# Kernel optimization log

Hardware: AMD Instinct MI355X
Metric: run time of the kernel (lower is better)

Reference implementation:

```python
import jax, jax.numpy as jnp
import numpy as np

N_NODES = 100000
N_HYPEREDGES = 10000
NNZ = 1600000

def setup_inputs() -> dict:
    key = jax.random.key(0)
    k = jax.random.split(key, 7)
    return {
        "x": jax.random.normal(k[0], (N_NODES, 1), dtype=jnp.float32),
        "W1": jax.random.normal(k[1], (1, 128), dtype=jnp.float32) * 0.5,
        "b1": jax.random.normal(k[2], (128,), dtype=jnp.float32) * 0.1,
        "W2": jax.random.normal(k[3], (128, 1), dtype=jnp.float32) * 0.1,
        "b2": jax.random.normal(k[4], (1,), dtype=jnp.float32) * 0.1,
        "node_idx": jax.random.randint(k[5], (NNZ,), 0, N_NODES, dtype=jnp.int64),
        "edge_idx": jax.random.randint(k[6], (NNZ,), 0, N_HYPEREDGES, dtype=jnp.int64),
    }

def _hypergraph_conv(x, W, b, node_idx, edge_idx, n_nodes, n_edges):
    # PyG HypergraphConv (use_attention=False, hyperedge_weight=1):
    # out = D^-1 H B^-1 H^T (X W) + b
    x = x @ W  # [N, F_out]
    ones = jnp.ones(node_idx.shape[0], dtype=x.dtype)
    D = jax.ops.segment_sum(ones, node_idx, num_segments=n_nodes)   # node degree
    B = jax.ops.segment_sum(ones, edge_idx, num_segments=n_edges)   # hyperedge degree
    D_inv = jnp.where(D > 0, 1.0 / D, 0.0)
    B_inv = jnp.where(B > 0, 1.0 / B, 0.0)
    # node -> hyperedge: e = B^-1 H^T x
    e = B_inv[:, None] * jax.ops.segment_sum(x[node_idx], edge_idx, num_segments=n_edges)
    # hyperedge -> node: out = D^-1 H e
    out = D_inv[:, None] * jax.ops.segment_sum(e[edge_idx], node_idx, num_segments=n_nodes)
    return out + b

def reference(x, W1, b1, W2, b2, node_idx, edge_idx):
    n_nodes = x.shape[0]
    h = _hypergraph_conv(x, W1, b1, node_idx, edge_idx, n_nodes, N_HYPEREDGES)
    h = jax.nn.relu(h)
    out = _hypergraph_conv(h, W2, b2, node_idx, edge_idx, n_nodes, N_HYPEREDGES)
    return out
```

## Files before the change

kernel.cpp:

```cpp
#include <hip/hip_runtime.h>

static constexpr int N_NODES = 100000;
static constexpr int N_EDGES = 10000;
static constexpr int NNZ     = 1600000;

static constexpr int G1    = 256;
static constexpr int CHUNK = NNZ / G1;
static constexpr int NRN   = 250;
static constexpr int RN    = 400;
static constexpr int NRE   = 250;
static constexpr int RE    = 40;
static constexpr int SLOT  = 64;
static constexpr int BLK   = 1024;
static constexpr int NW    = BLK / 64;
static constexpr int GF    = 250;
static constexpr int NBAR  = 8;
static constexpr int BARSTRIDE = 32;


__device__ __forceinline__ float ld_a(const float* p) {
    return __hip_atomic_load(p, __ATOMIC_RELAXED, __HIP_MEMORY_SCOPE_AGENT);
}
__device__ __forceinline__ void st_a(float* p, float v) {
    __hip_atomic_store(p, v, __ATOMIC_RELAXED, __HIP_MEMORY_SCOPE_AGENT);
}

__device__ __forceinline__ void grid_barrier(unsigned* bar, int phase) {
    __syncthreads();
    if (threadIdx.x == 0) {
        unsigned* cnt = bar + (size_t)phase * NBAR * BARSTRIDE;
        __hip_atomic_fetch_add(cnt + (blockIdx.x & (NBAR - 1)) * BARSTRIDE, 1u,
                               __ATOMIC_RELAXED, __HIP_MEMORY_SCOPE_AGENT);
        unsigned sum;
        do {
            __builtin_amdgcn_s_sleep(2);
            sum = 0u;
            #pragma unroll
            for (int g = 0; g < NBAR; ++g)
                sum += __hip_atomic_load(cnt + g * BARSTRIDE,
                                         __ATOMIC_RELAXED, __HIP_MEMORY_SCOPE_AGENT);
        } while (sum < (unsigned)GF);
    }
    __syncthreads();
}

__global__ __launch_bounds__(BLK) void k_bin(
        const int* __restrict__ nidx, const int* __restrict__ eidx,
        unsigned* __restrict__ binN, unsigned* __restrict__ binE,
        unsigned* __restrict__ cntN, unsigned* __restrict__ cntE,
        unsigned* __restrict__ bar) {
    __shared__ unsigned cN[NRN], cE[NRE];
    if (blockIdx.x == 0 && threadIdx.x < 3 * NBAR * BARSTRIDE) bar[threadIdx.x] = 0u;
    for (int j = threadIdx.x; j < NRN; j += BLK) cN[j] = 0u;
    for (int j = threadIdx.x; j < NRE; j += BLK) cE[j] = 0u;
    __syncthreads();
    const int b = blockIdx.x;
    const int i0 = b * CHUNK, i1 = i0 + CHUNK;
    for (int i = i0 + threadIdx.x; i < i1; i += BLK) {
        int n = nidx[i], e = eidx[i];
        int rn = n / RN;
        int re = e / RE;
        unsigned pn = atomicAdd(&cN[rn], 1u);
        unsigned pe = atomicAdd(&cE[re], 1u);
        binN[((size_t)rn * G1 + b) * SLOT + pn] = ((unsigned)(n - rn * RN) << 14) | (unsigned)e;
        binE[((size_t)re * G1 + b) * SLOT + pe] = ((unsigned)(e - re * RE) << 17) | (unsigned)n;
    }
    __syncthreads();
    for (int j = threadIdx.x; j < NRN; j += BLK) cntN[(size_t)j * G1 + b] = cN[j];
    for (int j = threadIdx.x; j < NRE; j += BLK) cntE[(size_t)j * G1 + b] = cE[j];
}

__global__ __launch_bounds__(BLK) void k_fused(
        const unsigned* __restrict__ binN, const unsigned* __restrict__ binE,
        const unsigned* __restrict__ cntN, const unsigned* __restrict__ cntE,
        const float* __restrict__ x,
        const float* __restrict__ W1, const float* __restrict__ b1,
        const float* __restrict__ W2, const float* __restrict__ b2,
        float* __restrict__ v1, float* __restrict__ v2, float* __restrict__ y,
        unsigned* __restrict__ bar, float* __restrict__ out) {
    __shared__ union {
        struct { unsigned scnt[G1]; float sS[NW][RE]; unsigned sC[NW][RE]; } e;
        struct { float sV[N_EDGES]; float sS[RN]; unsigned sC[RN]; unsigned scnt[G1];
                 float wgt[384]; } n;
    } sm;
    const int b = blockIdx.x;
    const int t = threadIdx.x;

    float my_binv = 0.0f;
    float my_dinv = 0.0f;

    {
        for (int j = t; j < NW * RE; j += BLK) { (&sm.e.sS[0][0])[j] = 0.0f; (&sm.e.sC[0][0])[j] = 0u; }
        if (t < G1) sm.e.scnt[t] = cntE[(size_t)b * G1 + t];
        __syncthreads();
        const int wv = t >> 6;
        const unsigned* base = binE + (size_t)b * G1 * SLOT;
        for (int j = t; j < G1 * SLOT; j += BLK) {
            int s = j & (SLOT - 1), bb = j >> 6;
            if ((unsigned)s < sm.e.scnt[bb]) {
                unsigned w = base[j];
                atomicAdd(&sm.e.sS[wv][w >> 17], x[w & 0x1FFFFu]);
                atomicAdd(&sm.e.sC[wv][w >> 17], 1u);
            }
        }
        __syncthreads();
        if (t < RE) {
            float s = 0.0f; unsigned c = 0u;
            #pragma unroll
            for (int k = 0; k < NW; ++k) { s += sm.e.sS[k][t]; c += sm.e.sC[k][t]; }
            my_binv = (c > 0u) ? (1.0f / (float)c) : 0.0f;
            st_a(&v1[b * RE + t], s * my_binv);
        }
    }
    grid_barrier(bar, 0);

    {
        for (int j = t; j < N_EDGES; j += BLK) sm.n.sV[j] = ld_a(&v1[j]);
        if (t < RN) { sm.n.sS[t] = 0.0f; sm.n.sC[t] = 0u; }
        if (t < G1) sm.n.scnt[t] = cntN[(size_t)b * G1 + t];
        if (t < 128) {
            sm.n.wgt[t]       = W1[t];
            sm.n.wgt[128 + t] = b1[t];
            sm.n.wgt[256 + t] = W2[t];
        }
        __syncthreads();
        const unsigned* base = binN + (size_t)b * G1 * SLOT;
        for (int j = t; j < G1 * SLOT; j += BLK) {
            int s = j & (SLOT - 1), bb = j >> 6;
            if ((unsigned)s < sm.n.scnt[bb]) {
                unsigned w = base[j];
                unsigned nl = w >> 14;
                atomicAdd(&sm.n.sS[nl], sm.n.sV[w & 0x3FFFu]);
                atomicAdd(&sm.n.sC[nl], 1u);
            }
        }
        __syncthreads();
        if (t < RN) {
            unsigned c = sm.n.sC[t];
            my_dinv = (c > 0u) ? (1.0f / (float)c) : 0.0f;
            float tt = sm.n.sS[t] * my_dinv;
            float acc = 0.0f;
            #pragma unroll
            for (int f = 0; f < 128; ++f) {
                float h = fmaf(tt, sm.n.wgt[f], sm.n.wgt[128 + f]);
                h = fmaxf(h, 0.0f);
                acc = fmaf(h, sm.n.wgt[256 + f], acc);
            }
            st_a(&y[b * RN + t], acc);
        }
    }
    grid_barrier(bar, 1);

    {
        for (int j = t; j < NW * RE; j += BLK) (&sm.e.sS[0][0])[j] = 0.0f;
        if (t < G1) sm.e.scnt[t] = cntE[(size_t)b * G1 + t];
        __syncthreads();
        const int wv = t >> 6;
        const unsigned* base = binE + (size_t)b * G1 * SLOT;
        for (int j = t; j < G1 * SLOT; j += BLK) {
            int s = j & (SLOT - 1), bb = j >> 6;
            if ((unsigned)s < sm.e.scnt[bb]) {
                unsigned w = base[j];
                atomicAdd(&sm.e.sS[wv][w >> 17], ld_a(&y[w & 0x1FFFFu]));
            }
        }
        __syncthreads();
        if (t < RE) {
            float s = 0.0f;
            #pragma unroll
            for (int k = 0; k < NW; ++k) s += sm.e.sS[k][t];
            st_a(&v2[b * RE + t], s * my_binv);
        }
    }
    grid_barrier(bar, 2);

    {
        for (int j = t; j < N_EDGES; j += BLK) sm.n.sV[j] = ld_a(&v2[j]);
        if (t < RN) sm.n.sS[t] = 0.0f;
        if (t < G1) sm.n.scnt[t] = cntN[(size_t)b * G1 + t];
        __syncthreads();
        const unsigned* base = binN + (size_t)b * G1 * SLOT;
        for (int j = t; j < G1 * SLOT; j += BLK) {
            int s = j & (SLOT - 1), bb = j >> 6;
            if ((unsigned)s < sm.n.scnt[bb]) {
                unsigned w = base[j];
                atomicAdd(&sm.n.sS[w >> 14], sm.n.sV[w & 0x3FFFu]);
            }
        }
        __syncthreads();
        if (t < RN) {
            out[b * RN + t] = fmaf(sm.n.sS[t], my_dinv, b2[0]);
        }
    }
}

extern "C" void kernel_launch(void* const* d_in, const int* in_sizes, int n_in,
                              void* d_out, int out_size, void* d_ws, size_t ws_size,
                              hipStream_t stream) {
    const float* x    = (const float*)d_in[0];
    const float* W1   = (const float*)d_in[1];
    const float* b1   = (const float*)d_in[2];
    const float* W2   = (const float*)d_in[3];
    const float* b2   = (const float*)d_in[4];
    const int*   nidx = (const int*)d_in[5];
    const int*   eidx = (const int*)d_in[6];
    float*       out  = (float*)d_out;

    char* ws = (char*)d_ws;
    unsigned* binN = (unsigned*)(ws + 0);
    unsigned* binE = (unsigned*)(ws + 16384000);
    unsigned* cntN = (unsigned*)(ws + 32768000);
    unsigned* cntE = (unsigned*)(ws + 33024000);
    float*    v1   = (float*)(ws + 33280000);
    float*    y    = (float*)(ws + 33320000);
    float*    v2   = (float*)(ws + 33720000);
    unsigned* bar  = (unsigned*)(ws + 33760000);

    k_bin  <<<G1, BLK, 0, stream>>>(nidx, eidx, binN, binE, cntN, cntE, bar);
    k_fused<<<GF, BLK, 0, stream>>>(binN, binE, cntN, cntE, x, W1, b1, W2, b2,
                                    v1, v2, y, bar, out);
}
```

Before: 88.46 us.

## Compute layer-2 edge sums from node-side partials and split barrier arrive/wait

The layer-2 node-to-edge aggregation no longer reads y from global memory through the edge bins. Each block now scatters its local y values into a per-block partial array over all 10000 edges in shared memory, writes it to global memory, and after a barrier each block reduces its 40 edges' partials across the 250 blocks. The grid barrier is split into an arrive step and a wait step, so setup work overlaps the wait, and a single master block sets a flag that the other blocks poll. This avoids the random global gathers of y, at the cost of a 10 MB partial-sum write and read and a serialized flag-based release.

```diff
diff --git a/kernel.cpp b/kernel.cpp
--- a/kernel.cpp
+++ b/kernel.cpp
@@ -12,10 +12,8 @@
 static constexpr int RE    = 40;
 static constexpr int SLOT  = 64;
 static constexpr int BLK   = 1024;
-static constexpr int NW    = BLK / 64;
+static constexpr int NW    = 16;
 static constexpr int GF    = 250;
-static constexpr int NBAR  = 8;
-static constexpr int BARSTRIDE = 32;
 
 
 __device__ __forceinline__ float ld_a(const float* p) {
@@ -25,21 +23,32 @@
     __hip_atomic_store(p, v, __ATOMIC_RELAXED, __HIP_MEMORY_SCOPE_AGENT);
 }
 
-__device__ __forceinline__ void grid_barrier(unsigned* bar, int phase) {
-    __syncthreads();
+__device__ __forceinline__ void bar_arrive(unsigned* bar, int phase) {
+    __syncthreads();
+    if (threadIdx.x == 0)
+        __hip_atomic_fetch_add(bar + phase * 256 + (blockIdx.x & 7) * 32, 1u,
+                               __ATOMIC_RELAXED, __HIP_MEMORY_SCOPE_AGENT);
+}
+__device__ __forceinline__ void bar_wait(unsigned* bar, int phase) {
     if (threadIdx.x == 0) {
-        unsigned* cnt = bar + (size_t)phase * NBAR * BARSTRIDE;
-        __hip_atomic_fetch_add(cnt + (blockIdx.x & (NBAR - 1)) * BARSTRIDE, 1u,
-                               __ATOMIC_RELAXED, __HIP_MEMORY_SCOPE_AGENT);
-        unsigned sum;
-        do {
-            __builtin_amdgcn_s_sleep(2);
-            sum = 0u;
-            #pragma unroll
-            for (int g = 0; g < NBAR; ++g)
-                sum += __hip_atomic_load(cnt + g * BARSTRIDE,
-                                         __ATOMIC_RELAXED, __HIP_MEMORY_SCOPE_AGENT);
-        } while (sum < (unsigned)GF);
+        unsigned* flag = bar + 768 + phase * 32;
+        if (blockIdx.x == 0) {
+            unsigned* cnt = bar + phase * 256;
+            unsigned sum;
+            do {
+                __builtin_amdgcn_s_sleep(2);
+                sum = 0u;
+                #pragma unroll
+                for (int g = 0; g < 8; ++g)
+                    sum += __hip_atomic_load(cnt + g * 32, __ATOMIC_RELAXED,
+                                             __HIP_MEMORY_SCOPE_AGENT);
+            } while (sum < (unsigned)GF);
+            __hip_atomic_store(flag, 1u, __ATOMIC_RELAXED, __HIP_MEMORY_SCOPE_AGENT);
+        } else {
+            while (__hip_atomic_load(flag, __ATOMIC_RELAXED,
+                                     __HIP_MEMORY_SCOPE_AGENT) == 0u)
+                __builtin_amdgcn_s_sleep(2);
+        }
     }
     __syncthreads();
 }
@@ -50,7 +59,7 @@
         unsigned* __restrict__ cntN, unsigned* __restrict__ cntE,
         unsigned* __restrict__ bar) {
     __shared__ unsigned cN[NRN], cE[NRE];
-    if (blockIdx.x == 0 && threadIdx.x < 3 * NBAR * BARSTRIDE) bar[threadIdx.x] = 0u;
+    if (blockIdx.x == 0 && threadIdx.x < 896) bar[threadIdx.x] = 0u;
     for (int j = threadIdx.x; j < NRN; j += BLK) cN[j] = 0u;
     for (int j = threadIdx.x; j < NRE; j += BLK) cE[j] = 0u;
     __syncthreads();
@@ -76,122 +85,126 @@
         const float* __restrict__ x,
         const float* __restrict__ W1, const float* __restrict__ b1,
         const float* __restrict__ W2, const float* __restrict__ b2,
-        float* __restrict__ v1, float* __restrict__ v2, float* __restrict__ y,
+        float* __restrict__ v1, float* __restrict__ v2, float* __restrict__ P_S,
         unsigned* __restrict__ bar, float* __restrict__ out) {
-    __shared__ union {
-        struct { unsigned scnt[G1]; float sS[NW][RE]; unsigned sC[NW][RE]; } e;
-        struct { float sV[N_EDGES]; float sS[RN]; unsigned sC[RN]; unsigned scnt[G1];
-                 float wgt[384]; } n;
-    } sm;
+    __shared__ float    sBig[N_EDGES];
+    __shared__ float    eS[NW][RE];
+    __shared__ unsigned eC[NW][RE];
+    __shared__ float    sS_n[RN];
+    __shared__ unsigned sC_n[RN];
+    __shared__ unsigned scntE[G1];
+    __shared__ unsigned scntN[G1];
+    __shared__ float    wgt[384];
+    __shared__ float    y_loc[RN];
+
     const int b = blockIdx.x;
     const int t = threadIdx.x;
-
+    const int wv = t >> 6;
     float my_binv = 0.0f;
     float my_dinv = 0.0f;
 
+    for (int j = t; j < NW * RE; j += BLK) { (&eS[0][0])[j] = 0.0f; (&eC[0][0])[j] = 0u; }
+    if (t < G1) scntE[t] = cntE[(size_t)b * G1 + t];
+    __syncthreads();
     {
-        for (int j = t; j < NW * RE; j += BLK) { (&sm.e.sS[0][0])[j] = 0.0f; (&sm.e.sC[0][0])[j] = 0u; }
-        if (t < G1) sm.e.scnt[t] = cntE[(size_t)b * G1 + t];
-        __syncthreads();
-        const int wv = t >> 6;
-        const unsigned* base = binE + (size_t)b * G1 * SLOT;
+        const unsigned* baseE = binE + (size_t)b * G1 * SLOT;
         for (int j = t; j < G1 * SLOT; j += BLK) {
             int s = j & (SLOT - 1), bb = j >> 6;
-            if ((unsigned)s < sm.e.scnt[bb]) {
-                unsigned w = base[j];
-                atomicAdd(&sm.e.sS[wv][w >> 17], x[w & 0x1FFFFu]);
-                atomicAdd(&sm.e.sC[wv][w >> 17], 1u);
+            if ((unsigned)s < scntE[bb]) {
+                unsigned w = baseE[j];
+                atomicAdd(&eS[wv][w >> 17], x[w & 0x1FFFFu]);
+                atomicAdd(&eC[wv][w >> 17], 1u);
             }
         }
         __syncthreads();
         if (t < RE) {
             float s = 0.0f; unsigned c = 0u;
             #pragma unroll
-            for (int k = 0; k < NW; ++k) { s += sm.e.sS[k][t]; c += sm.e.sC[k][t]; }
+            for (int k = 0; k < NW; ++k) { s += eS[k][t]; c += eC[k][t]; }
             my_binv = (c > 0u) ? (1.0f / (float)c) : 0.0f;
             st_a(&v1[b * RE + t], s * my_binv);
         }
     }
-    grid_barrier(bar, 0);
-
+    bar_arrive(bar, 0);
+    if (t < RN) { sS_n[t] = 0.0f; sC_n[t] = 0u; }
+    if (t < G1) scntN[t] = cntN[(size_t)b * G1 + t];
+    if (t < 128) { wgt[t] = W1[t]; wgt[128 + t] = b1[t]; wgt[256 + t] = W2[t]; }
+    bar_wait(bar, 0);
+
+    const unsigned* baseN = binN + (size_t)b * G1 * SLOT;
+    for (int j = t; j < N_EDGES; j += BLK) sBig[j] = ld_a(&v1[j]);
+    __syncthreads();
+    for (int j = t; j < G1 * SLOT; j += BLK) {
+        int s = j & (SLOT - 1), bb = j >> 6;
+        if ((unsigned)s < scntN[bb]) {
+            unsigned w = baseN[j];
+            atomicAdd(&sS_n[w >> 14], sBig[w & 0x3FFFu]);
+            atomicAdd(&sC_n[w >> 14], 1u);
+        }
+    }
+    __syncthreads();
+    if (t < RN) {
+        unsigned c = sC_n[t];
+        my_dinv = (c > 0u) ? (1.0f / (float)c) : 0.0f;
+        float tt = sS_n[t] * my_dinv;
+        float acc = 0.0f;
+        #pragma unroll
+        for (int f = 0; f < 128; ++f) {
+            float h = fmaf(tt, wgt[f], wgt[128 + f]);
+            h = fmaxf(h, 0.0f);
+            acc = fmaf(h, wgt[256 + f], acc);
+        }
+        y_loc[t] = acc;
+    }
+    __syncthreads();
+    for (int j = t; j < N_EDGES; j += BLK) sBig[j] = 0.0f;
+    __syncthreads();
+    for (int j = t; j < G1 * SLOT; j += BLK) {
+        int s = j & (SLOT - 1), bb = j >> 6;
+        if ((unsigned)s < scntN[bb]) {
+            unsigned w = baseN[j];
+            atomicAdd(&sBig[w & 0x3FFFu], y_loc[w >> 14]);
+        }
+    }
+    __syncthreads();
     {
-        for (int j = t; j < N_EDGES; j += BLK) sm.n.sV[j] = ld_a(&v1[j]);
-        if (t < RN) { sm.n.sS[t] = 0.0f; sm.n.sC[t] = 0u; }
-        if (t < G1) sm.n.scnt[t] = cntN[(size_t)b * G1 + t];
-        if (t < 128) {
-            sm.n.wgt[t]       = W1[t];
-            sm.n.wgt[128 + t] = b1[t];
-            sm.n.wgt[256 + t] = W2[t];
-        }
-        __syncthreads();
-        const unsigned* base = binN + (size_t)b * G1 * SLOT;
-        for (int j = t; j < G1 * SLOT; j += BLK) {
-            int s = j & (SLOT - 1), bb = j >> 6;
-            if ((unsigned)s < sm.n.scnt[bb]) {
-                unsigned w = base[j];
-                unsigned nl = w >> 14;
-                atomicAdd(&sm.n.sS[nl], sm.n.sV[w & 0x3FFFu]);
-                atomicAdd(&sm.n.sC[nl], 1u);
-            }
-        }
-        __syncthreads();
-        if (t < RN) {
-            unsigned c = sm.n.sC[t];
-            my_dinv = (c > 0u) ? (1.0f / (float)c) : 0.0f;
-            float tt = sm.n.sS[t] * my_dinv;
+        float* ps = P_S + (size_t)b * N_EDGES;
+        for (int j = t; j < N_EDGES; j += BLK) st_a(&ps[j], sBig[j]);
+    }
+    bar_arrive(bar, 1);
+    bar_wait(bar, 1);
+
+    {
+        const int lane = t & 63;
+        if (lane < RE) {
             float acc = 0.0f;
-            #pragma unroll
-            for (int f = 0; f < 128; ++f) {
-                float h = fmaf(tt, sm.n.wgt[f], sm.n.wgt[128 + f]);
-                h = fmaxf(h, 0.0f);
-                acc = fmaf(h, sm.n.wgt[256 + f], acc);
-            }
-            st_a(&y[b * RN + t], acc);
-        }
-    }
-    grid_barrier(bar, 1);
-
-    {
-        for (int j = t; j < NW * RE; j += BLK) (&sm.e.sS[0][0])[j] = 0.0f;
-        if (t < G1) sm.e.scnt[t] = cntE[(size_t)b * G1 + t];
-        __syncthreads();
-        const int wv = t >> 6;
-        const unsigned* base = binE + (size_t)b * G1 * SLOT;
-        for (int j = t; j < G1 * SLOT; j += BLK) {
-            int s = j & (SLOT - 1), bb = j >> 6;
-            if ((unsigned)s < sm.e.scnt[bb]) {
-                unsigned w = base[j];
-                atomicAdd(&sm.e.sS[wv][w >> 17], ld_a(&y[w & 0x1FFFFu]));
-            }
-        }
-        __syncthreads();
-        if (t < RE) {
-            float s = 0.0f;
-            #pragma unroll
-            for (int k = 0; k < NW; ++k) s += sm.e.sS[k][t];
-            st_a(&v2[b * RE + t], s * my_binv);
-        }
-    }
-    grid_barrier(bar, 2);
-
-    {
-        for (int j = t; j < N_EDGES; j += BLK) sm.n.sV[j] = ld_a(&v2[j]);
-        if (t < RN) sm.n.sS[t] = 0.0f;
-        if (t < G1) sm.n.scnt[t] = cntN[(size_t)b * G1 + t];
-        __syncthreads();
-        const unsigned* base = binN + (size_t)b * G1 * SLOT;
-        for (int j = t; j < G1 * SLOT; j += BLK) {
-            int s = j & (SLOT - 1), bb = j >> 6;
-            if ((unsigned)s < sm.n.scnt[bb]) {
-                unsigned w = base[j];
-                atomicAdd(&sm.n.sS[w >> 14], sm.n.sV[w & 0x3FFFu]);
-            }
-        }
-        __syncthreads();
-        if (t < RN) {
-            out[b * RN + t] = fmaf(sm.n.sS[t], my_dinv, b2[0]);
-        }
-    }
+            for (int g = wv; g < GF; g += NW)
+                acc += ld_a(&P_S[(size_t)g * N_EDGES + b * RE + lane]);
+            eS[wv][lane] = acc;
+        }
+    }
+    __syncthreads();
+    if (t < RE) {
+        float s = 0.0f;
+        #pragma unroll
+        for (int k = 0; k < NW; ++k) s += eS[k][t];
+        st_a(&v2[b * RE + t], s * my_binv);
+    }
+    bar_arrive(bar, 2);
+    if (t < RN) sS_n[t] = 0.0f;
+    bar_wait(bar, 2);
+
+    for (int j = t; j < N_EDGES; j += BLK) sBig[j] = ld_a(&v2[j]);
+    __syncthreads();
+    for (int j = t; j < G1 * SLOT; j += BLK) {
+        int s = j & (SLOT - 1), bb = j >> 6;
+        if ((unsigned)s < scntN[bb]) {
+            unsigned w = baseN[j];
+            atomicAdd(&sS_n[w >> 14], sBig[w & 0x3FFFu]);
+        }
+    }
+    __syncthreads();
+    if (t < RN) out[b * RN + t] = fmaf(sS_n[t], my_dinv, b2[0]);
 }
 
 extern "C" void kernel_launch(void* const* d_in, const int* in_sizes, int n_in,
@@ -212,11 +225,11 @@
     unsigned* cntN = (unsigned*)(ws + 32768000);
     unsigned* cntE = (unsigned*)(ws + 33024000);
     float*    v1   = (float*)(ws + 33280000);
-    float*    y    = (float*)(ws + 33320000);
-    float*    v2   = (float*)(ws + 33720000);
-    unsigned* bar  = (unsigned*)(ws + 33760000);
+    float*    v2   = (float*)(ws + 33320000);
+    float*    P_S  = (float*)(ws + 33360000);
+    unsigned* bar  = (unsigned*)(ws + 43360000);
 
     k_bin  <<<G1, BLK, 0, stream>>>(nidx, eidx, binN, binE, cntN, cntE, bar);
     k_fused<<<GF, BLK, 0, stream>>>(binN, binE, cntN, cntE, x, W1, b1, W2, b2,
-                                    v1, v2, y, bar, out);
-}
+                                    v1, v2, P_S, bar, out);
+}
```

After: 85.01 us. 1.04x faster.
